# Kernel tuning notes

Measured on AMD Instinct MI355X. Metric: run time of the kernel, lower is better.

Reference implementation:

```python
import jax, jax.numpy as jnp
import numpy as np


def _conv1x1_relu(x, W, b):
    # x: (B, Cin, N, k), W: (Cout, Cin), b: (Cout,) -> (B, Cout, N, k)
    return jax.nn.relu(jnp.einsum('bcnk,oc->bonk', x, W) + b[None, :, None, None])


def _knn_idx(pc, k):
    # pc: (B, C, N). Mirrors torch: dis_mat = -||pi - pj||^2, topk (largest) -> nearest.
    G = jnp.einsum('bcn,bcm->bnm', pc, pc)            # (B, N, N)
    sq = jnp.sum(pc * pc, axis=1)                      # (B, N)
    neg_dist = 2.0 * G - sq[:, :, None] - sq[:, None, :]
    _, idx = jax.lax.top_k(neg_dist, k)                # (B, N, k) int32
    return idx


def _group_points(x, idx):
    # x: (B, C, N), idx: (B, N, k) -> (B, C, N, k); out[b,c,n,j] = x[b,c,idx[b,n,j]]
    B, C, N = x.shape
    k = idx.shape[-1]
    idx2 = jnp.broadcast_to(idx.reshape(B, 1, N * k), (B, C, N * k))
    return jnp.take_along_axis(x, idx2, axis=2).reshape(B, C, N, k)


def setup_inputs() -> dict:
    key = jax.random.key(0)
    ks = jax.random.split(key, 8)
    B, N, C, O, K = 8, 4096, 64, 64, 16
    s = 0.05
    return {
        'xyz': jax.random.normal(ks[0], (B, 3, N), dtype=jnp.float32),
        'fea': jax.random.normal(ks[1], (B, C, N), dtype=jnp.float32),
        'Wg1': jax.random.normal(ks[2], (O, 10), dtype=jnp.float32) * s,
        'bg1': jnp.zeros((O,), dtype=jnp.float32),
        'Wg2': jax.random.normal(ks[3], (O, O), dtype=jnp.float32) * s,
        'bg2': jnp.zeros((O,), dtype=jnp.float32),
        'Wf1': jax.random.normal(ks[4], (O, 2 * C), dtype=jnp.float32) * s,
        'bf1': jnp.zeros((O,), dtype=jnp.float32),
        'Wf2': jax.random.normal(ks[5], (O, O), dtype=jnp.float32) * s,
        'bf2': jnp.zeros((O,), dtype=jnp.float32),
        'Wf3': jax.random.normal(ks[6], (O, O), dtype=jnp.float32) * s,
        'bf3': jnp.zeros((O,), dtype=jnp.float32),
        'k': 16,
    }


def reference(xyz, fea, Wg1, bg1, Wg2, bg2, Wf1, bf1, Wf2, bf2, Wf3, bf3, k):
    idx = _knn_idx(fea, k)                             # (B, N, k)

    # get_edge_point: (B, 10, N, k)
    xyz_knn = _group_points(xyz, idx)                  # (B, 3, N, k)
    xyz_c = jnp.broadcast_to(xyz[:, :, :, None], xyz_knn.shape)
    xyz_r = xyz_c - xyz_knn
    xyz_d = jnp.sqrt(jnp.sum(xyz_r * xyz_r, axis=1, keepdims=True))
    geo = jnp.concatenate([xyz_d, xyz_c, xyz_knn, xyz_r], axis=1)

    # get_edge_feature: (B, 2C, N, k)
    fea_knn = _group_points(fea, idx)
    fea_c = jnp.broadcast_to(fea[:, :, :, None], fea_knn.shape)
    edge = jnp.concatenate([fea_c, fea_knn], axis=1)

    g = _conv1x1_relu(geo, Wg1, bg1)
    g = _conv1x1_relu(g, Wg2, bg2)

    f = _conv1x1_relu(edge, Wf1, bf1)
    f = _conv1x1_relu(f, Wf2, bf2)
    f = _conv1x1_relu(f, Wf3, bf3)

    out = jnp.max(g * f, axis=-1)                      # (B, O, N)
    return out
```

## Files before the change

kernel.cpp:

```cpp
#include <hip/hip_runtime.h>
#include <math.h>

#define NB 8
#define NPTS 4096
#define NCH 64
#define NOUT 64
#define KNN 16

#define GLOBAL_AS const __attribute__((address_space(1)))
#define LDS_AS __attribute__((address_space(3)))

#define WS_SQ  0
#define WS_PT  (NB*NPTS)
#define WS_QT  (WS_PT + NB*NPTS*64)
#define WS_IDX (WS_QT + NB*NPTS*64)

__global__ __launch_bounds__(256) void k_sq(const float* __restrict__ fea,
                                            float* __restrict__ sq) {
    int g = blockIdx.x * 256 + threadIdx.x;
    int b = g >> 12, n = g & 4095;
    const float* f = fea + (size_t)b * NCH * NPTS + n;
    float s = 0.f;
#pragma unroll
    for (int c = 0; c < NCH; ++c) s = fmaf(f[c * NPTS], f[c * NPTS], s);
    sq[g] = s;
}

__global__ __launch_bounds__(256, 2) void k_knn(const float* __restrict__ fea,
                                                const float* __restrict__ sq,
                                                int* __restrict__ idxout) {
    __shared__ __align__(16) float rowT[64][64];
    __shared__ __align__(16) float colT[2][64 * 128];

    const int b = blockIdx.y;
    const int n0 = blockIdx.x * 64;
    const int tid = threadIdx.x;
    const int lane = tid & 63, w = tid >> 6;
    const int g = lane >> 4, p = lane & 15;
    const int rbase = w * 16 + g * 4;
    const float* feab = fea + (size_t)b * NCH * NPTS;

    auto stage_async = [&](int buf, int m0) {
#pragma unroll
        for (int i = 0; i < 8; ++i) {
            int k = w * 8 + i;
            int c = 2 * k + (lane >> 5);
            int j = (lane & 31) * 4;
            const float* gp = feab + c * NPTS + m0 + j;
            float* lp = &colT[buf][k * 256];
            __builtin_amdgcn_global_load_lds((GLOBAL_AS void*)gp,
                                             (LDS_AS void*)lp, 16, 0, 0);
        }
    };

#pragma unroll
    for (int i = 0; i < 4; ++i) {
        int e = i * 1024 + tid * 4;
        int c = e >> 6, r = e & 63;
        *(float4*)&rowT[c][r] = *(const float4*)&feab[c * NPTS + n0 + r];
    }
    stage_async(0, 0);

    float lstv[4];
    int   lsti[4];
    float thr[4];
#pragma unroll
    for (int i = 0; i < 4; ++i) {
        lstv[i] = -3.0e38f; lsti[i] = 0; thr[i] = -3.0e38f;
    }

    auto ins = [&](int i, float vv, int col) {
        unsigned long long lt = __ballot(lstv[i] < vv);
        int pos = __popc((unsigned)((lt >> (g * 16)) & 0xFFFFull));
        float nv = __shfl_down(lstv[i], 1, 16);
        int   ni = __shfl_down(lsti[i], 1, 16);
        if (p <= pos - 2)      { lstv[i] = nv; lsti[i] = ni; }
        else if (p == pos - 1) { lstv[i] = vv; lsti[i] = col; }
    };

    __syncthreads();

    for (int t = 0; t < 32; ++t) {
        const int m0 = t * 128;
        const int cur = t & 1;
        if (t < 31) stage_async(cur ^ 1, m0 + 128);

        float4 sql = *(const float4*)&sq[b * NPTS + m0 + p * 4];
        float4 sqh = *(const float4*)&sq[b * NPTS + m0 + 64 + p * 4];

        float acc[4][8];
#pragma unroll
        for (int i = 0; i < 4; ++i)
#pragma unroll
            for (int j = 0; j < 8; ++j) acc[i][j] = 0.f;

#pragma unroll 4
        for (int c = 0; c < 64; ++c) {
            float4 rv  = *(const float4*)&rowT[c][rbase];
            float4 cv0 = *(const float4*)&colT[cur][c * 128 + p * 4];
            float4 cv1 = *(const float4*)&colT[cur][c * 128 + 64 + p * 4];
            float rr[4] = {rv.x, rv.y, rv.z, rv.w};
            float c0[4] = {cv0.x, cv0.y, cv0.z, cv0.w};
            float c1[4] = {cv1.x, cv1.y, cv1.z, cv1.w};
#pragma unroll
            for (int ri = 0; ri < 4; ++ri) {
#pragma unroll
                for (int cj = 0; cj < 4; ++cj) {
                    acc[ri][cj]     = fmaf(rr[ri], c0[cj], acc[ri][cj]);
                    acc[ri][cj + 4] = fmaf(rr[ri], c1[cj], acc[ri][cj + 4]);
                }
            }
        }

        float sqa[8] = {sql.x, sql.y, sql.z, sql.w, sqh.x, sqh.y, sqh.z, sqh.w};
#pragma unroll
        for (int i = 0; i < 4; ++i)
#pragma unroll
            for (int j = 0; j < 8; ++j)
                acc[i][j] = fmaf(2.f, acc[i][j], -sqa[j]);

#pragma unroll
        for (int i = 0; i < 4; ++i) {
#pragma unroll
            for (int h = 0; h < 2; ++h) {
                float v0 = acc[i][h * 4 + 0], v1 = acc[i][h * 4 + 1];
                float v2 = acc[i][h * 4 + 2], v3 = acc[i][h * 4 + 3];
                float vm = fmaxf(fmaxf(v0, v1), fmaxf(v2, v3));
                unsigned long long bal = __ballot(vm > thr[i]);
                unsigned mg = (unsigned)((bal >> (g * 16)) & 0xFFFFull);
                while (__any(mg != 0u)) {
                    bool act = (mg != 0u);
                    int srcp = act ? (__ffs(mg) - 1) : 0;
                    mg &= (mg - 1u);
                    int srcl = (g << 4) | srcp;
                    float b0 = __shfl(v0, srcl);
                    float b1 = __shfl(v1, srcl);
                    float b2 = __shfl(v2, srcl);
                    float b3 = __shfl(v3, srcl);
                    if (act) {
                        int cb = m0 + h * 64 + srcp * 4;
                        if (b0 > thr[i]) ins(i, b0, cb + 0);
                        if (b1 > thr[i]) ins(i, b1, cb + 1);
                        if (b2 > thr[i]) ins(i, b2, cb + 2);
                        if (b3 > thr[i]) ins(i, b3, cb + 3);
                    }
                }
                if (bal) thr[i] = __shfl(lstv[i], 0, 16);
            }
        }
        __syncthreads();
    }

#pragma unroll
    for (int i = 0; i < 4; ++i) {
        int row = rbase + i;
        idxout[((size_t)(b * NPTS) + n0 + row) * KNN + (15 - p)] = lsti[i];
    }
}

__global__ __launch_bounds__(256) void k_pq(const float* __restrict__ fea,
                                            const float* __restrict__ Wf1,
                                            const float* __restrict__ bf1,
                                            float* __restrict__ Pt,
                                            float* __restrict__ Qt) {
    __shared__ __align__(16) float feaT[64][64];
    __shared__ __align__(16) float WT[64][132];
    __shared__ float sb[64];

    const int b = blockIdx.y;
    const int n0 = blockIdx.x * 64;
    const int tid = threadIdx.x;
    const int to = tid & 15, tn = tid >> 4;
    const float* feab = fea + (size_t)b * NCH * NPTS;

#pragma unroll
    for (int i = 0; i < 4; ++i) {
        int e = i * 1024 + tid * 4;
        int c = e >> 6, nn = e & 63;
        *(float4*)&feaT[c][nn] = *(const float4*)&feab[c * NPTS + n0 + nn];
    }
#pragma unroll
    for (int i = 0; i < 8; ++i) {
        int g = tid * 32 + i * 4;
        int op = g >> 6, c = g & 63;
        const float* src = (op < 64) ? &Wf1[op * 128 + c]
                                     : &Wf1[(op - 64) * 128 + 64 + c];
        float4 w = *(const float4*)src;
        WT[c + 0][op] = w.x; WT[c + 1][op] = w.y;
        WT[c + 2][op] = w.z; WT[c + 3][op] = w.w;
    }
    if (tid < 64) sb[tid] = bf1[tid];
    __syncthreads();

    float acc[4][8];
#pragma unroll
    for (int ni = 0; ni < 4; ++ni)
#pragma unroll
        for (int oj = 0; oj < 8; ++oj) acc[ni][oj] = 0.f;

#pragma unroll 4
    for (int c = 0; c < 64; ++c) {
        float4 a  = *(const float4*)&feaT[c][tn * 4];
        float4 w0 = *(const float4*)&WT[c][to * 8];
        float4 w1 = *(const float4*)&WT[c][to * 8 + 4];
        float av[4] = {a.x, a.y, a.z, a.w};
        float wv[8] = {w0.x, w0.y, w0.z, w0.w, w1.x, w1.y, w1.z, w1.w};
#pragma unroll
        for (int ni = 0; ni < 4; ++ni)
#pragma unroll
            for (int oj = 0; oj < 8; ++oj)
                acc[ni][oj] = fmaf(av[ni], wv[oj], acc[ni][oj]);
    }

    const int opb = to * 8;
#pragma unroll
    for (int ni = 0; ni < 4; ++ni) {
        int n = n0 + tn * 4 + ni;
        size_t base = ((size_t)b * NPTS + n) * 64;
        if (opb < 64) {
            float4 o0, o1;
            o0.x = acc[ni][0] + sb[opb + 0]; o0.y = acc[ni][1] + sb[opb + 1];
            o0.z = acc[ni][2] + sb[opb + 2]; o0.w = acc[ni][3] + sb[opb + 3];
            o1.x = acc[ni][4] + sb[opb + 4]; o1.y = acc[ni][5] + sb[opb + 5];
            o1.z = acc[ni][6] + sb[opb + 6]; o1.w = acc[ni][7] + sb[opb + 7];
            *(float4*)&Pt[base + opb]     = o0;
            *(float4*)&Pt[base + opb + 4] = o1;
        } else {
            float4 o0, o1;
            o0.x = acc[ni][0]; o0.y = acc[ni][1]; o0.z = acc[ni][2]; o0.w = acc[ni][3];
            o1.x = acc[ni][4]; o1.y = acc[ni][5]; o1.z = acc[ni][6]; o1.w = acc[ni][7];
            *(float4*)&Qt[base + opb - 64]     = o0;
            *(float4*)&Qt[base + opb - 64 + 4] = o1;
        }
    }
}

__global__ __launch_bounds__(256) void k_mlp(
    const float* __restrict__ xyz,
    const float* __restrict__ Pt, const float* __restrict__ Qt,
    const int* __restrict__ knnidx,
    const float* __restrict__ Wg1, const float* __restrict__ bg1,
    const float* __restrict__ Wg2, const float* __restrict__ bg2,
    const float* __restrict__ Wf2, const float* __restrict__ bf2,
    const float* __restrict__ Wf3, const float* __restrict__ bf3,
    float* __restrict__ out) {
    __shared__ __align__(16) float bufX[64][68];
    __shared__ __align__(16) float bufY[64][68];
    __shared__ __align__(16) float Wbuf[64][68];
    __shared__ __align__(16) float scratch[1280];
    __shared__ float biasS[64];
    __shared__ int sidx[64];

    const int b = blockIdx.y;
    const int n0 = blockIdx.x * 4;
    const int tid = threadIdx.x;
    const int to = tid & 15, tp = tid >> 4;

    if (tid < 64)
        sidx[tid] = knnidx[((size_t)(b * NPTS + n0)) * KNN + tid];
    __syncthreads();

    {
        int pair = tid >> 2, q = tid & 3;
        int m = sidx[pair];
        int pt = pair >> 4;
        const float* pB = &Pt[((size_t)b * NPTS + n0 + pt) * 64];
        const float* qB = &Qt[((size_t)b * NPTS + m) * 64];
#pragma unroll
        for (int i = 0; i < 4; ++i) {
            int c0 = q * 16 + i * 4;
            float4 pv = *(const float4*)&pB[c0];
            float4 qv = *(const float4*)&qB[c0];
            bufX[c0 + 0][pair] = fmaxf(pv.x + qv.x, 0.f);
            bufX[c0 + 1][pair] = fmaxf(pv.y + qv.y, 0.f);
            bufX[c0 + 2][pair] = fmaxf(pv.z + qv.z, 0.f);
            bufX[c0 + 3][pair] = fmaxf(pv.w + qv.w, 0.f);
        }
    }
    if (tid < 64) {
        int pair = tid, pt = pair >> 4;
        int m = sidx[pair];
        const float* xb = xyz + (size_t)b * 3 * NPTS;
        float cx = xb[0 * NPTS + n0 + pt], cy = xb[1 * NPTS + n0 + pt], cz = xb[2 * NPTS + n0 + pt];
        float kx = xb[0 * NPTS + m], ky = xb[1 * NPTS + m], kz = xb[2 * NPTS + m];
        float rx = cx - kx, ry = cy - ky, rz = cz - kz;
        float d = sqrtf(rx * rx + ry * ry + rz * rz);
        scratch[0 * 68 + pair] = d;
        scratch[1 * 68 + pair] = cx; scratch[2 * 68 + pair] = cy; scratch[3 * 68 + pair] = cz;
        scratch[4 * 68 + pair] = kx; scratch[5 * 68 + pair] = ky; scratch[6 * 68 + pair] = kz;
        scratch[7 * 68 + pair] = rx; scratch[8 * 68 + pair] = ry; scratch[9 * 68 + pair] = rz;
    }

    auto stageW = [&](const float* W, const float* bv) {
#pragma unroll
        for (int i = 0; i < 4; ++i) {
            int g = tid * 16 + i * 4;
            int o = g >> 6, c = g & 63;
            float4 w = *(const float4*)&W[g];
            Wbuf[c + 0][o] = w.x; Wbuf[c + 1][o] = w.y;
            Wbuf[c + 2][o] = w.z; Wbuf[c + 3][o] = w.w;
        }
        if (tid < 64) biasS[tid] = bv[tid];
    };

    auto gemmPh = [&](const float* src, float* dst, int Kdim) {
        float acc[4][4] = {{0.f,0.f,0.f,0.f},{0.f,0.f,0.f,0.f},
                           {0.f,0.f,0.f,0.f},{0.f,0.f,0.f,0.f}};
#pragma unroll 2
        for (int c = 0; c < Kdim; ++c) {
            float4 w = *(const float4*)&Wbuf[c][to * 4];
            float4 a = *(const float4*)(src + c * 68 + tp * 4);
            float wr[4] = {w.x, w.y, w.z, w.w};
            float ar[4] = {a.x, a.y, a.z, a.w};
#pragma unroll
            for (int oi = 0; oi < 4; ++oi)
#pragma unroll
                for (int pj = 0; pj < 4; ++pj)
                    acc[oi][pj] = fmaf(wr[oi], ar[pj], acc[oi][pj]);
        }
#pragma unroll
        for (int oi = 0; oi < 4; ++oi) {
            float bo = biasS[to * 4 + oi];
            float4 o4;
            o4.x = fmaxf(acc[oi][0] + bo, 0.f);
            o4.y = fmaxf(acc[oi][1] + bo, 0.f);
            o4.z = fmaxf(acc[oi][2] + bo, 0.f);
            o4.w = fmaxf(acc[oi][3] + bo, 0.f);
            *(float4*)(dst + (to * 4 + oi) * 68 + tp * 4) = o4;
        }
    };

    stageW(Wf2, bf2);
    __syncthreads();
    gemmPh(&bufX[0][0], &bufY[0][0], 64);
    __syncthreads();
    stageW(Wf3, bf3);
    __syncthreads();
    gemmPh(&bufY[0][0], &bufX[0][0], 64);
    __syncthreads();
    {
        for (int e = tid; e < 640; e += 256) {
            int o = e / 10, c = e - o * 10;
            Wbuf[c][o] = Wg1[e];
        }
        if (tid < 64) biasS[tid] = bg1[tid];
    }
    __syncthreads();
    gemmPh(scratch, &bufY[0][0], 10);
    __syncthreads();
    stageW(Wg2, bg2);
    __syncthreads();
    {
        float acc[4][4] = {{0.f,0.f,0.f,0.f},{0.f,0.f,0.f,0.f},
                           {0.f,0.f,0.f,0.f},{0.f,0.f,0.f,0.f}};
#pragma unroll 2
        for (int c = 0; c < 64; ++c) {
            float4 w = *(const float4*)&Wbuf[c][to * 4];
            float4 a = *(const float4*)&bufY[c][tp * 4];
            float wr[4] = {w.x, w.y, w.z, w.w};
            float ar[4] = {a.x, a.y, a.z, a.w};
#pragma unroll
            for (int oi = 0; oi < 4; ++oi)
#pragma unroll
                for (int pj = 0; pj < 4; ++pj)
                    acc[oi][pj] = fmaf(wr[oi], ar[pj], acc[oi][pj]);
        }
#pragma unroll
        for (int oi = 0; oi < 4; ++oi) {
            int o = to * 4 + oi;
            float bo = biasS[o];
            float mx = -3.0e38f;
#pragma unroll
            for (int pj = 0; pj < 4; ++pj) {
                float g2v = fmaxf(acc[oi][pj] + bo, 0.f);
                float f3v = bufX[o][tp * 4 + pj];
                mx = fmaxf(mx, g2v * f3v);
            }
            scratch[o * 17 + tp] = mx;
        }
    }
    __syncthreads();
    {
        int o = tid & 63, pt = tid >> 6;
        float m0_ = scratch[o * 17 + pt * 4 + 0];
        float m1  = scratch[o * 17 + pt * 4 + 1];
        float m2  = scratch[o * 17 + pt * 4 + 2];
        float m3  = scratch[o * 17 + pt * 4 + 3];
        out[((size_t)b * 64 + o) * NPTS + n0 + pt] =
            fmaxf(fmaxf(m0_, m1), fmaxf(m2, m3));
    }
}

extern "C" void kernel_launch(void* const* d_in, const int* in_sizes, int n_in,
                              void* d_out, int out_size, void* d_ws, size_t ws_size,
                              hipStream_t stream) {
    const float* xyz = (const float*)d_in[0];
    const float* fea = (const float*)d_in[1];
    const float* Wg1 = (const float*)d_in[2];
    const float* bg1 = (const float*)d_in[3];
    const float* Wg2 = (const float*)d_in[4];
    const float* bg2 = (const float*)d_in[5];
    const float* Wf1 = (const float*)d_in[6];
    const float* bf1 = (const float*)d_in[7];
    const float* Wf2 = (const float*)d_in[8];
    const float* bf2 = (const float*)d_in[9];
    const float* Wf3 = (const float*)d_in[10];
    const float* bf3 = (const float*)d_in[11];
    float* out = (float*)d_out;
    float* ws = (float*)d_ws;

    float* sq = ws + WS_SQ;
    float* Pt = ws + WS_PT;
    float* Qt = ws + WS_QT;
    int* idxw = (int*)(ws + WS_IDX);

    k_sq <<<dim3(128),      dim3(256), 0, stream>>>(fea, sq);
    k_knn<<<dim3(64, 8),    dim3(256), 0, stream>>>(fea, sq, idxw);
    k_pq <<<dim3(64, 8),    dim3(256), 0, stream>>>(fea, Wf1, bf1, Pt, Qt);
    k_mlp<<<dim3(1024, 8),  dim3(256), 0, stream>>>(xyz, Pt, Qt, idxw,
                                                    Wg1, bg1, Wg2, bg2,
                                                    Wf2, bf2, Wf3, bf3, out);
}
```

Before: 734.7 us.

## Split KNN candidates into two halves, enlarge row tile, merge partial top-k lists

The KNN kernel now gives each block 128 query rows with an 8x8 register tile per thread and scans only half of the candidate columns. The two halves each produce a sorted top-16 list, and a new merge kernel combines them. This raises FMA reuse per LDS load and keeps the block count about the same. The column buffer is now single-buffered with a sync after each stage, so loads no longer overlap compute, and the list-shift shuffle is replaced with a DPP row shift. The change costs an extra kernel launch and the writes of the partial lists, and register pressure rises with 8 rows per thread under a 2-wave occupancy bound.

```diff
diff --git a/kernel.cpp b/kernel.cpp
--- a/kernel.cpp
+++ b/kernel.cpp
@@ -6,6 +6,7 @@
 #define NCH 64
 #define NOUT 64
 #define KNN 16
+#define HALFC 2048
 
 #define GLOBAL_AS const __attribute__((address_space(1)))
 #define LDS_AS __attribute__((address_space(3)))
@@ -28,99 +29,99 @@
 
 __global__ __launch_bounds__(256, 2) void k_knn(const float* __restrict__ fea,
                                                 const float* __restrict__ sq,
-                                                int* __restrict__ idxout) {
-    __shared__ __align__(16) float rowT[64][64];
-    __shared__ __align__(16) float colT[2][64 * 128];
-
-    const int b = blockIdx.y;
-    const int n0 = blockIdx.x * 64;
+                                                float* __restrict__ vh,
+                                                int* __restrict__ ih) {
+    __shared__ __align__(16) float rowT[64][128];
+    __shared__ __align__(16) float colT[64 * 128];
+
+    const int b = blockIdx.z;
+    const int half = blockIdx.y;
+    const int n0 = blockIdx.x * 128;
+    const int cbase = half * HALFC;
     const int tid = threadIdx.x;
     const int lane = tid & 63, w = tid >> 6;
     const int g = lane >> 4, p = lane & 15;
-    const int rbase = w * 16 + g * 4;
+    const int rbase = w * 32 + g * 8;
     const float* feab = fea + (size_t)b * NCH * NPTS;
 
-    auto stage_async = [&](int buf, int m0) {
+    auto stage = [&](int m0) {
 #pragma unroll
         for (int i = 0; i < 8; ++i) {
             int k = w * 8 + i;
             int c = 2 * k + (lane >> 5);
             int j = (lane & 31) * 4;
             const float* gp = feab + c * NPTS + m0 + j;
-            float* lp = &colT[buf][k * 256];
+            float* lp = &colT[k * 256];
             __builtin_amdgcn_global_load_lds((GLOBAL_AS void*)gp,
                                              (LDS_AS void*)lp, 16, 0, 0);
         }
     };
 
 #pragma unroll
-    for (int i = 0; i < 4; ++i) {
+    for (int i = 0; i < 8; ++i) {
         int e = i * 1024 + tid * 4;
-        int c = e >> 6, r = e & 63;
+        int c = e >> 7, r = e & 127;
         *(float4*)&rowT[c][r] = *(const float4*)&feab[c * NPTS + n0 + r];
     }
-    stage_async(0, 0);
-
-    float lstv[4];
-    int   lsti[4];
-    float thr[4];
-#pragma unroll
-    for (int i = 0; i < 4; ++i) {
+
+    float lstv[8];
+    int   lsti[8];
+    float thr[8];
+#pragma unroll
+    for (int i = 0; i < 8; ++i) {
         lstv[i] = -3.0e38f; lsti[i] = 0; thr[i] = -3.0e38f;
     }
 
     auto ins = [&](int i, float vv, int col) {
         unsigned long long lt = __ballot(lstv[i] < vv);
-        int pos = __popc((unsigned)((lt >> (g * 16)) & 0xFFFFull));
-        float nv = __shfl_down(lstv[i], 1, 16);
-        int   ni = __shfl_down(lsti[i], 1, 16);
-        if (p <= pos - 2)      { lstv[i] = nv; lsti[i] = ni; }
+        int pos = __popc((unsigned)((lt >> (g * 16)) & 0xFFFFu));
+        int nv = __builtin_amdgcn_update_dpp(0, __float_as_int(lstv[i]),
+                                             0x101, 0xF, 0xF, true);
+        int ni = __builtin_amdgcn_update_dpp(0, lsti[i],
+                                             0x101, 0xF, 0xF, true);
+        if (p <= pos - 2)      { lstv[i] = __int_as_float(nv); lsti[i] = ni; }
         else if (p == pos - 1) { lstv[i] = vv; lsti[i] = col; }
     };
 
-    __syncthreads();
-
-    for (int t = 0; t < 32; ++t) {
-        const int m0 = t * 128;
-        const int cur = t & 1;
-        if (t < 31) stage_async(cur ^ 1, m0 + 128);
+    for (int t = 0; t < 16; ++t) {
+        const int m0 = cbase + t * 128;
+        stage(m0);
+        __syncthreads();
 
         float4 sql = *(const float4*)&sq[b * NPTS + m0 + p * 4];
         float4 sqh = *(const float4*)&sq[b * NPTS + m0 + 64 + p * 4];
 
-        float acc[4][8];
-#pragma unroll
-        for (int i = 0; i < 4; ++i)
+        float acc[8][8];
+#pragma unroll
+        for (int i = 0; i < 8; ++i)
 #pragma unroll
             for (int j = 0; j < 8; ++j) acc[i][j] = 0.f;
 
-#pragma unroll 4
+#pragma unroll 2
         for (int c = 0; c < 64; ++c) {
-            float4 rv  = *(const float4*)&rowT[c][rbase];
-            float4 cv0 = *(const float4*)&colT[cur][c * 128 + p * 4];
-            float4 cv1 = *(const float4*)&colT[cur][c * 128 + 64 + p * 4];
-            float rr[4] = {rv.x, rv.y, rv.z, rv.w};
-            float c0[4] = {cv0.x, cv0.y, cv0.z, cv0.w};
-            float c1[4] = {cv1.x, cv1.y, cv1.z, cv1.w};
-#pragma unroll
-            for (int ri = 0; ri < 4; ++ri) {
-#pragma unroll
-                for (int cj = 0; cj < 4; ++cj) {
-                    acc[ri][cj]     = fmaf(rr[ri], c0[cj], acc[ri][cj]);
-                    acc[ri][cj + 4] = fmaf(rr[ri], c1[cj], acc[ri][cj + 4]);
-                }
-            }
-        }
-
-        float sqa[8] = {sql.x, sql.y, sql.z, sql.w, sqh.x, sqh.y, sqh.z, sqh.w};
-#pragma unroll
-        for (int i = 0; i < 4; ++i)
+            float4 ra = *(const float4*)&rowT[c][rbase];
+            float4 rb = *(const float4*)&rowT[c][rbase + 4];
+            float4 ca = *(const float4*)&colT[c * 128 + p * 4];
+            float4 cb = *(const float4*)&colT[c * 128 + 64 + p * 4];
+            float rr[8] = {ra.x, ra.y, ra.z, ra.w, rb.x, rb.y, rb.z, rb.w};
+            float cc[8] = {ca.x, ca.y, ca.z, ca.w, cb.x, cb.y, cb.z, cb.w};
+#pragma unroll
+            for (int ri = 0; ri < 8; ++ri)
+#pragma unroll
+                for (int cj = 0; cj < 8; ++cj)
+                    acc[ri][cj] = fmaf(rr[ri], cc[cj], acc[ri][cj]);
+        }
+
+        float sqa[8] = {sql.x, sql.y, sql.z, sql.w,
+                        sqh.x, sqh.y, sqh.z, sqh.w};
+#pragma unroll
+        for (int i = 0; i < 8; ++i)
 #pragma unroll
             for (int j = 0; j < 8; ++j)
                 acc[i][j] = fmaf(2.f, acc[i][j], -sqa[j]);
 
 #pragma unroll
-        for (int i = 0; i < 4; ++i) {
+        for (int i = 0; i < 8; ++i) {
 #pragma unroll
             for (int h = 0; h < 2; ++h) {
                 float v0 = acc[i][h * 4 + 0], v1 = acc[i][h * 4 + 1];
@@ -152,9 +153,29 @@
     }
 
 #pragma unroll
-    for (int i = 0; i < 4; ++i) {
+    for (int i = 0; i < 8; ++i) {
         int row = rbase + i;
-        idxout[((size_t)(b * NPTS) + n0 + row) * KNN + (15 - p)] = lsti[i];
+        size_t base = ((size_t)(b * NPTS) + n0 + row) * 32 + half * 16;
+        vh[base + (15 - p)] = lstv[i];
+        ih[base + (15 - p)] = lsti[i];
+    }
+}
+
+__global__ __launch_bounds__(256) void k_merge(const float* __restrict__ vh,
+                                               const int* __restrict__ ih,
+                                               int* __restrict__ idxout) {
+    int row = blockIdx.x * 256 + threadIdx.x;
+    const float* v = vh + (size_t)row * 32;
+    const int* ii = ih + (size_t)row * 32;
+    size_t ob = (size_t)row * KNN;
+    int i0 = 0, i1 = 0;
+#pragma unroll
+    for (int j = 0; j < KNN; ++j) {
+        float v0 = (i0 < 16) ? v[i0] : -3.4e38f;
+        float v1 = (i1 < 16) ? v[16 + i1] : -3.4e38f;
+        bool t0 = (v0 >= v1);
+        idxout[ob + j] = t0 ? ii[i0] : ii[16 + i1];
+        if (t0) ++i0; else ++i1;
     }
 }
 
@@ -413,11 +434,14 @@
     float* Pt = ws + WS_PT;
     float* Qt = ws + WS_QT;
     int* idxw = (int*)(ws + WS_IDX);
-
-    k_sq <<<dim3(128),      dim3(256), 0, stream>>>(fea, sq);
-    k_knn<<<dim3(64, 8),    dim3(256), 0, stream>>>(fea, sq, idxw);
-    k_pq <<<dim3(64, 8),    dim3(256), 0, stream>>>(fea, Wf1, bf1, Pt, Qt);
-    k_mlp<<<dim3(1024, 8),  dim3(256), 0, stream>>>(xyz, Pt, Qt, idxw,
-                                                    Wg1, bg1, Wg2, bg2,
-                                                    Wf2, bf2, Wf3, bf3, out);
-}
+    float* vh = ws + WS_PT;
+    int*   ih = (int*)(ws + WS_PT + NB * NPTS * 32);
+
+    k_sq   <<<dim3(128),       dim3(256), 0, stream>>>(fea, sq);
+    k_knn  <<<dim3(32, 2, 8),  dim3(256), 0, stream>>>(fea, sq, vh, ih);
+    k_merge<<<dim3(128),       dim3(256), 0, stream>>>(vh, ih, idxw);
+    k_pq   <<<dim3(64, 8),     dim3(256), 0, stream>>>(fea, Wf1, bf1, Pt, Qt);
+    k_mlp  <<<dim3(1024, 8),   dim3(256), 0, stream>>>(xyz, Pt, Qt, idxw,
+                                                       Wg1, bg1, Wg2, bg2,
+                                                       Wf2, bf2, Wf3, bf3, out);
+}
```

Result: no change. 743.5 us (+1.2%).
